# Performance work log

Hardware: AMD Instinct MI355X
Metric: run time of the kernel (lower is better)

## Reference

```python
import jax, jax.numpy as jnp
import numpy as np

B, T, D_MODEL = 4, 1024, 1024
H, DQK, DV = 16, 64, 64
POS_NUM = 2 * T - 1  # 2047
SCALE = 0.05  # keep softmax logits in a sane range for random weights


def setup_inputs() -> dict:
    key = jax.random.key(0)
    ks = jax.random.split(key, 8)
    x = jax.random.normal(ks[0], (B, T, D_MODEL), dtype=jnp.float32)
    W_Q = jax.random.normal(ks[1], (H, DQK, DQK), dtype=jnp.float32) * SCALE
    W_K = jax.random.normal(ks[2], (H, DQK, DQK), dtype=jnp.float32) * SCALE
    W_V = jax.random.normal(ks[3], (H, DQK, DV), dtype=jnp.float32) * SCALE
    W_Z = jax.random.normal(ks[4], (H * DV, D_MODEL), dtype=jnp.float32) * SCALE
    pos_K_emb = jax.random.normal(ks[5], (POS_NUM, DQK), dtype=jnp.float32) * SCALE
    pos_V_emb = jax.random.normal(ks[6], (POS_NUM, DV), dtype=jnp.float32) * SCALE
    mask = jnp.zeros((T, T), dtype=jnp.float32)  # additive attention mask
    pos = jax.random.randint(ks[7], (T, T), 0, POS_NUM, dtype=jnp.int32)
    return {"x": x, "W_Q": W_Q, "W_K": W_K, "W_V": W_V, "W_Z": W_Z,
            "pos_K_emb": pos_K_emb, "pos_V_emb": pos_V_emb,
            "mask": mask, "pos": pos}


def reference(x, W_Q, W_K, W_V, W_Z, pos_K_emb, pos_V_emb, mask, pos):
    Bs, Ts, _ = x.shape
    h, dqk, dv = W_V.shape
    # [B,T,D] -> [B,H,T,dQK]
    xh = x.reshape(Bs, Ts, h, dqk).transpose(0, 2, 1, 3)
    Q = jnp.einsum('bhtd,hde->bhte', xh, W_Q)
    K = jnp.einsum('bhtd,hde->bhte', xh, W_K)
    V = jnp.einsum('bhtd,hde->bhte', xh, W_V)
    # content scores + relative-position key bias
    PK = pos_K_emb[pos]                       # [T,T,dQK]
    scores = jnp.einsum('bhqd,bhkd->bhqk', Q, K)
    scores = scores + jnp.einsum('bhqd,qkd->bhqk', Q, PK)
    # NOTE: original adds mask BEFORE dividing by sqrt(dQK); replicate exactly
    scores = (scores + mask) / jnp.sqrt(jnp.asarray(dqk, dtype=scores.dtype))
    attn = jax.nn.softmax(scores, axis=-1)    # [B,H,T,T]
    ctx = jnp.einsum('bhqk,bhkd->bhqd', attn, V)
    PV = pos_V_emb[pos]                       # [T,T,dV]
    ctx = ctx + jnp.einsum('bhqk,qkd->bhqd', attn, PV)
    out = ctx.transpose(0, 2, 1, 3).reshape(Bs, Ts, h * dv)
    return out @ W_Z
```

## Files before the change

### kernel.cpp

```cpp
#include <hip/hip_runtime.h>
#include <hip/hip_bf16.h>

#define BB 4
#define TT 1024
#define DM 1024
#define HH 16

typedef __attribute__((ext_vector_type(8))) short short8;
typedef __attribute__((ext_vector_type(4))) short short4v;
typedef __attribute__((ext_vector_type(4))) float f32x4;
typedef __hip_bfloat16 bf16;
typedef unsigned char u8;

__device__ __forceinline__ f32x4 mfma16(short8 a, short8 b, f32x4 c) {
  return __builtin_amdgcn_mfma_f32_16x16x32_bf16(a, b, c, 0, 0, 0);
}
__device__ __forceinline__ f32x4 mfma8(long a, long b, f32x4 c) {
  return __builtin_amdgcn_mfma_f32_16x16x32_fp8_fp8(a, b, c, 0, 0, 0);
}

__global__ __launch_bounds__(256) void xb_kernel(
    const float* __restrict__ x, bf16* __restrict__ xb) {
  const size_t i = ((size_t)blockIdx.x * 256 + threadIdx.x) * 8;
  bf16 tmp[8];
#pragma unroll
  for (int j = 0; j < 8; ++j) tmp[j] = __float2bfloat16(x[i + j]);
  *(short8*)(xb + i) = *(const short8*)tmp;
}

__global__ __launch_bounds__(256) void pack_pm_kernel(
    const int* __restrict__ pos, const float* __restrict__ maskp,
    unsigned* __restrict__ pm) {
  const size_t i = (size_t)blockIdx.x * 256 + threadIdx.x;
  const unsigned mb = __float_as_uint(maskp[i]) & 0xffff0000u;
  pm[i] = mb | (unsigned)pos[i];
}

__global__ __launch_bounds__(256) void prep_w_kernel(
    const float* __restrict__ WQ, const float* __restrict__ WK,
    const float* __restrict__ WV, bf16* __restrict__ Wt) {
  __shared__ bf16 tl[64][72];
  const int h = blockIdx.x, m = blockIdx.y;
  const float* W = (m == 0 ? WQ : (m == 1 ? WK : WV)) + h * 4096;
  const int tid = threadIdx.x;
  const int r = tid >> 2, c = (tid & 3) * 16;
#pragma unroll
  for (int i = 0; i < 16; ++i)
    tl[r][c + i] = __float2bfloat16(W[r * 64 + c + i]);
  __syncthreads();
  bf16* o = Wt + ((size_t)(m * 16 + h) * 64 + r) * 64 + c;
#pragma unroll
  for (int i = 0; i < 16; ++i) o[i] = tl[c + i][r];
}

__global__ __launch_bounds__(256) void prep_posk8_kernel(
    const float* __restrict__ posK, u8* __restrict__ posK8) {
  const int idx = (blockIdx.x * 256 + threadIdx.x) * 2;
  const int p = idx >> 6, d = idx & 63;
  const float v0 = (p < 2047) ? posK[(size_t)p * 64 + d] : 0.f;
  const float v1 = (p < 2047) ? posK[(size_t)p * 64 + d + 1] : 0.f;
  const int pk = __builtin_amdgcn_cvt_pk_fp8_f32(v0, v1, 0, false);
  *(unsigned short*)(posK8 + idx) = (unsigned short)(pk & 0xffff);
}

__global__ __launch_bounds__(256) void trans_wz_kernel(
    const float* __restrict__ Wz, bf16* __restrict__ WzT) {
  __shared__ bf16 tile[64][72];
  const int k0 = blockIdx.y * 64, n0 = blockIdx.x * 64;
  const int tid = threadIdx.x;
  const int r = tid >> 2, c = (tid & 3) * 16;
  const float* s = Wz + (size_t)(k0 + r) * 1024 + n0 + c;
#pragma unroll
  for (int i = 0; i < 16; ++i) tile[r][c + i] = __float2bfloat16(s[i]);
  __syncthreads();
  const int n = tid >> 2;
  bf16* o = WzT + (size_t)(n0 + n) * 1024 + k0 + c;
#pragma unroll
  for (int i = 0; i < 16; ++i) o[i] = tile[c + i][n];
}

__global__ __launch_bounds__(256) void trans_v_kernel(
    const bf16* __restrict__ src, bf16* __restrict__ dst) {
  __shared__ bf16 tile[64][72];
  const int bh = blockIdx.y, t0 = blockIdx.x * 64;
  const int tid = threadIdx.x;
  const int r = tid >> 2, c = (tid & 3) * 16;
  const bf16* s = src + ((size_t)bh * TT + t0 + r) * 64 + c;
  *(short8*)(&tile[r][c]) = *(const short8*)(s);
  *(short8*)(&tile[r][c + 8]) = *(const short8*)(s + 8);
  __syncthreads();
  const int d = tid >> 2;
  bf16* o = dst + ((size_t)bh * 64 + d) * TT + t0 + c;
#pragma unroll
  for (int i = 0; i < 16; ++i) o[i] = tile[c + i][d];
}

__global__ __launch_bounds__(256) void qkv_mfma_kernel(
    const bf16* __restrict__ xb, const bf16* __restrict__ Wt,
    u8* __restrict__ Q8, u8* __restrict__ K8, bf16* __restrict__ Vg) {
  __shared__ __align__(16) bf16 xs[64 * 72];
  const int bh = blockIdx.y;
  const int b = bh >> 4, h = bh & 15;
  const int t0 = blockIdx.x * 64;
  const int tid = threadIdx.x;
  const int w = tid >> 6, lane = tid & 63, l15 = lane & 15, hi = lane >> 4;

  {
    const int r = tid >> 2, c = (tid & 3) * 16;
    const bf16* src = xb + ((size_t)b * TT + t0 + r) * DM + h * 64 + c;
    *(short8*)(xs + r * 72 + c) = *(const short8*)(src);
    *(short8*)(xs + r * 72 + c + 8) = *(const short8*)(src + 8);
  }
  __syncthreads();

  f32x4 aQ[4] = {{0.f, 0.f, 0.f, 0.f}, {0.f, 0.f, 0.f, 0.f},
                 {0.f, 0.f, 0.f, 0.f}, {0.f, 0.f, 0.f, 0.f}};
  f32x4 aK[4] = {{0.f, 0.f, 0.f, 0.f}, {0.f, 0.f, 0.f, 0.f},
                 {0.f, 0.f, 0.f, 0.f}, {0.f, 0.f, 0.f, 0.f}};
  f32x4 aV[4] = {{0.f, 0.f, 0.f, 0.f}, {0.f, 0.f, 0.f, 0.f},
                 {0.f, 0.f, 0.f, 0.f}, {0.f, 0.f, 0.f, 0.f}};
  const bf16* WtQ = Wt + (size_t)h * 4096;
  const bf16* WtK = Wt + (size_t)(16 + h) * 4096;
  const bf16* WtV = Wt + (size_t)(32 + h) * 4096;
#pragma unroll
  for (int kc = 0; kc < 2; ++kc) {
    const short8 a =
        *(const short8*)(xs + (w * 16 + l15) * 72 + kc * 32 + hi * 8);
#pragma unroll
    for (int nt = 0; nt < 4; ++nt) {
      const size_t wo = (size_t)(nt * 16 + l15) * 64 + kc * 32 + hi * 8;
      aQ[nt] = mfma16(a, *(const short8*)(WtQ + wo), aQ[nt]);
      aK[nt] = mfma16(a, *(const short8*)(WtK + wo), aK[nt]);
      aV[nt] = mfma16(a, *(const short8*)(WtV + wo), aV[nt]);
    }
  }
  const int t = t0 + w * 16 + hi * 4;
#pragma unroll
  for (int nt = 0; nt < 4; ++nt) {
#pragma unroll
    for (int j = 0; j < 4; ++j) {
      const size_t o = ((size_t)bh * TT + t + j) * 64 + nt * 16 + l15;
      Vg[o] = __float2bfloat16(aV[nt][j]);
    }
    const size_t o0 = ((size_t)bh * TT + t) * 64 + nt * 16 + l15;
    {
      const int p01 = __builtin_amdgcn_cvt_pk_fp8_f32(aQ[nt][0], aQ[nt][1], 0, false);
      const int p23 = __builtin_amdgcn_cvt_pk_fp8_f32(aQ[nt][2], aQ[nt][3], 0, false);
      Q8[o0] = (u8)(p01 & 0xff);
      Q8[o0 + 64] = (u8)((p01 >> 8) & 0xff);
      Q8[o0 + 128] = (u8)(p23 & 0xff);
      Q8[o0 + 192] = (u8)((p23 >> 8) & 0xff);
    }
    {
      const int p01 = __builtin_amdgcn_cvt_pk_fp8_f32(aK[nt][0], aK[nt][1], 0, false);
      const int p23 = __builtin_amdgcn_cvt_pk_fp8_f32(aK[nt][2], aK[nt][3], 0, false);
      K8[o0] = (u8)(p01 & 0xff);
      K8[o0 + 64] = (u8)((p01 >> 8) & 0xff);
      K8[o0 + 128] = (u8)(p23 & 0xff);
      K8[o0 + 192] = (u8)((p23 >> 8) & 0xff);
    }
  }
}

#define QP8_S 2052
#define PSM_S 72

__global__ __launch_bounds__(256, 1) void score_pv_kernel(
    const u8* __restrict__ Q8,
    const u8* __restrict__ K8,
    const u8* __restrict__ posK8,
    const bf16* __restrict__ Vt,
    const unsigned* __restrict__ pm,
    bf16* __restrict__ Pws,
    float* __restrict__ l_ws,
    float* __restrict__ ctxU,
    int slab) {
  __shared__ __align__(16) u8 QPsh[64 * QP8_S];
  __shared__ __align__(16) bf16 Psm[2][64 * PSM_S];
  __shared__ float lred[4][64];

  const int bh = blockIdx.x;
  const int qt = blockIdx.y;
  const int qlocal0 = qt * 64;
  const int qg0 = slab * 256 + qlocal0;
  const int tid = threadIdx.x;
  const int w = tid >> 6;
  const int lane = tid & 63;
  const int l15 = lane & 15;
  const int hi = lane >> 4;

  long aqA[4], aqB[4];
#pragma unroll
  for (int h = 0; h < 4; ++h) {
    const u8* Qrow =
        Q8 + ((size_t)bh * TT + qg0 + h * 16 + l15) * 64;
    aqA[h] = *(const long*)(Qrow + hi * 8);
    aqB[h] = *(const long*)(Qrow + 32 + hi * 8);
  }

  {
    const u8* Kp0 = posK8 + (size_t)(w * 32 * 16 + l15) * 64;
    long qb0 = *(const long*)(Kp0 + hi * 8);
    long qb1 = *(const long*)(Kp0 + 32 + hi * 8);
    for (int i = 0; i < 32; ++i) {
      const int pt = w * 32 + i;
      const long cb0 = qb0, cb1 = qb1;
      {
        const int ptn = w * 32 + ((i + 1) & 31);
        const u8* Kpn = posK8 + (size_t)(ptn * 16 + l15) * 64;
        qb0 = *(const long*)(Kpn + hi * 8);
        qb1 = *(const long*)(Kpn + 32 + hi * 8);
      }
      const int off = pt * 16 + l15;
#pragma unroll
      for (int h = 0; h < 4; ++h) {
        f32x4 a4 = {0.f, 0.f, 0.f, 0.f};
        a4 = mfma8(aqA[h], cb0, a4);
        a4 = mfma8(aqB[h], cb1, a4);
        const int p01 = __builtin_amdgcn_cvt_pk_fp8_f32(a4[0], a4[1], 0, false);
        const int p23 = __builtin_amdgcn_cvt_pk_fp8_f32(a4[2], a4[3], 0, false);
        const int qr = h * 16 + hi * 4;
        QPsh[(qr + 0) * QP8_S + off] = (u8)(p01 & 0xff);
        QPsh[(qr + 1) * QP8_S + off] = (u8)((p01 >> 8) & 0xff);
        QPsh[(qr + 2) * QP8_S + off] = (u8)(p23 & 0xff);
        QPsh[(qr + 3) * QP8_S + off] = (u8)((p23 >> 8) & 0xff);
      }
    }
  }
  __syncthreads();

  f32x4 acc[4] = {{0.f, 0.f, 0.f, 0.f}, {0.f, 0.f, 0.f, 0.f},
                  {0.f, 0.f, 0.f, 0.f}, {0.f, 0.f, 0.f, 0.f}};
  float lp[16];
#pragma unroll
  for (int j = 0; j < 16; ++j) lp[j] = 0.f;
  const int kk = w * 16 + l15;
  const u8* K8bh = K8 + (size_t)bh * TT * 64;
  const bf16* Vtrow = Vt + ((size_t)bh * 64 + w * 16 + l15) * TT;

  long nb0 = *(const long*)(K8bh + (size_t)kk * 64 + hi * 8);
  long nb1 = *(const long*)(K8bh + (size_t)kk * 64 + 32 + hi * 8);
  short8 nv0 = *(const short8*)(Vtrow + hi * 8);
  short8 nv1 = *(const short8*)(Vtrow + 32 + hi * 8);
  unsigned npm[16];
#pragma unroll
  for (int h = 0; h < 4; ++h)
#pragma unroll
    for (int j = 0; j < 4; ++j)
      npm[h * 4 + j] = pm[(size_t)(qg0 + h * 16 + hi * 4 + j) * TT + kk];

  for (int it = 0; it < 16; ++it) {
    const int k0 = it * 64;
    bf16* PsmC = &Psm[it & 1][0];
    const long cb0 = nb0, cb1 = nb1;
    const short8 cv0 = nv0, cv1 = nv1;
    unsigned cpm[16];
#pragma unroll
    for (int j = 0; j < 16; ++j) cpm[j] = npm[j];
    {
      const int k0n = ((it + 1) & 15) * 64;
      nb0 = *(const long*)(K8bh + (size_t)(k0n + kk) * 64 + hi * 8);
      nb1 = *(const long*)(K8bh + (size_t)(k0n + kk) * 64 + 32 + hi * 8);
      nv0 = *(const short8*)(Vtrow + k0n + hi * 8);
      nv1 = *(const short8*)(Vtrow + k0n + 32 + hi * 8);
#pragma unroll
      for (int h = 0; h < 4; ++h)
#pragma unroll
        for (int j = 0; j < 4; ++j)
          npm[h * 4 + j] =
              pm[(size_t)(qg0 + h * 16 + hi * 4 + j) * TT + k0n + kk];
    }
#pragma unroll
    for (int h = 0; h < 4; ++h) {
      f32x4 s = {0.f, 0.f, 0.f, 0.f};
      s = mfma8(aqA[h], cb0, s);
      s = mfma8(aqB[h], cb1, s);
#pragma unroll
      for (int j = 0; j < 4; ++j) {
        const int q = h * 16 + hi * 4 + j;
        const unsigned pmv = cpm[h * 4 + j];
        const float qp = __builtin_amdgcn_cvt_f32_fp8(
            (int)QPsh[q * QP8_S + (pmv & 0xffffu)], 0);
        const float sv =
            (s[j] + qp + __uint_as_float(pmv & 0xffff0000u)) * 0.125f;
        const float pe = __expf(sv);
        lp[h * 4 + j] += pe;
        PsmC[q * PSM_S + kk] = __float2bfloat16(pe);
      }
    }
    __syncthreads();
    {
      const int r = tid >> 2, c = (tid & 3) * 16;
      *(short8*)(Pws + ((size_t)(qlocal0 + r) * 64 + bh) * TT + k0 + c) =
          *(const short8*)(PsmC + r * PSM_S + c);
      *(short8*)(Pws + ((size_t)(qlocal0 + r) * 64 + bh) * TT + k0 + c + 8) =
          *(const short8*)(PsmC + r * PSM_S + c + 8);
    }
#pragma unroll
    for (int h = 0; h < 4; ++h) {
      const short8 pa0 =
          *(const short8*)(PsmC + (h * 16 + l15) * PSM_S + hi * 8);
      acc[h] = mfma16(pa0, cv0, acc[h]);
      const short8 pa1 =
          *(const short8*)(PsmC + (h * 16 + l15) * PSM_S + 32 + hi * 8);
      acc[h] = mfma16(pa1, cv1, acc[h]);
    }
  }

#pragma unroll
  for (int j = 0; j < 16; ++j) {
    float v = lp[j];
    v += __shfl_xor(v, 1);
    v += __shfl_xor(v, 2);
    v += __shfl_xor(v, 4);
    v += __shfl_xor(v, 8);
    lp[j] = v;
  }
  __syncthreads();
  if (l15 == 0) {
#pragma unroll
    for (int h = 0; h < 4; ++h)
#pragma unroll
      for (int j = 0; j < 4; ++j) lred[w][h * 16 + hi * 4 + j] = lp[h * 4 + j];
  }
  __syncthreads();
  if (tid < 64) {
    const float l = lred[0][tid] + lred[1][tid] + lred[2][tid] + lred[3][tid];
    l_ws[(size_t)bh * TT + qg0 + tid] = l;
  }
  {
    const int b = bh >> 4, h16 = bh & 15;
#pragma unroll
    for (int h = 0; h < 4; ++h)
#pragma unroll
      for (int j = 0; j < 4; ++j) {
        const int q = h * 16 + hi * 4 + j;
        ctxU[((size_t)b * TT + qg0 + q) * DM + h16 * 64 + w * 16 + l15] =
            acc[h][j];
      }
  }
}

#define PVT_S 72
__global__ __launch_bounds__(256) void pv_part_kernel(
    const bf16* __restrict__ Pws,
    const float* __restrict__ posV,
    const unsigned* __restrict__ pm,
    float* __restrict__ PP,
    int slab) {
  __shared__ __align__(16) bf16 PVt[2][64 * PVT_S];
  __shared__ unsigned short possh[256];

  const int qlocal = blockIdx.x;
  const int q = slab * 256 + qlocal;
  const int ks = blockIdx.y;
  const int kbase = ks * 256;
  const int tid = threadIdx.x;
  const int w = tid >> 6, lane = tid & 63, l15 = lane & 15, hi = lane >> 4;

  possh[tid] = (unsigned short)(pm[(size_t)q * TT + kbase + tid] & 0xffffu);
  __syncthreads();

  f32x4 acc[4] = {{0.f, 0.f, 0.f, 0.f}, {0.f, 0.f, 0.f, 0.f},
                  {0.f, 0.f, 0.f, 0.f}, {0.f, 0.f, 0.f, 0.f}};
  const bf16* Prow = Pws + ((size_t)qlocal * 64 + w * 16 + l15) * TT;

  for (int it = 0; it < 4; ++it) {
    const int k0 = kbase + it * 64;
    bf16* pvt = &PVt[it & 1][0];
    {
      const int kr = lane;
      const int dc = w * 16;
      const int p = possh[it * 64 + kr];
      const float* src = posV + (size_t)p * 64 + dc;
#pragma unroll
      for (int ii = 0; ii < 16; ii += 4) {
        const f32x4 v = *(const f32x4*)(src + ii);
        pvt[(dc + ii + 0) * PVT_S + kr] = __float2bfloat16(v[0]);
        pvt[(dc + ii + 1) * PVT_S + kr] = __float2bfloat16(v[1]);
        pvt[(dc + ii + 2) * PVT_S + kr] = __float2bfloat16(v[2]);
        pvt[(dc + ii + 3) * PVT_S + kr] = __float2bfloat16(v[3]);
      }
    }
    __syncthreads();
#pragma unroll
    for (int kc = 0; kc < 2; ++kc) {
      const short8 a = *(const short8*)(Prow + k0 + kc * 32 + hi * 8);
#pragma unroll
      for (int nt = 0; nt < 4; ++nt) {
        const short8 bv =
            *(const short8*)(pvt + (nt * 16 + l15) * PVT_S + kc * 32 + hi * 8);
        acc[nt] = mfma16(a, bv, acc[nt]);
      }
    }
  }

  const int bh0 = w * 16 + hi * 4;
#pragma unroll
  for (int j = 0; j < 4; ++j) {
    const int bh = bh0 + j;
    float* o = PP + (((size_t)ks * 256 + qlocal) * 64 + bh) * 64;
#pragma unroll
    for (int nt = 0; nt < 4; ++nt) o[nt * 16 + l15] = acc[nt][j];
  }
}

__global__ __launch_bounds__(256) void norm_kernel(
    const float* __restrict__ PP,
    const float* __restrict__ ctxU,
    const float* __restrict__ l_ws,
    bf16* __restrict__ ctxB,
    int slab) {
  const int i4 = blockIdx.x * 256 + threadIdx.x;
  const int e0 = i4 * 4;
  const int dm = e0 & 1023;
  const int qlocal = (e0 >> 10) & 255;
  const int b = e0 >> 18;
  const int h = dm >> 6, d0 = dm & 63;
  const int bh = b * 16 + h;
  const int q = slab * 256 + qlocal;

  f32x4 v = *(const f32x4*)(ctxU + ((size_t)b * TT + q) * DM + dm);
#pragma unroll
  for (int ks = 0; ks < 4; ++ks)
    v += *(const f32x4*)(PP + (((size_t)ks * 256 + qlocal) * 64 + bh) * 64 + d0);
  const float invl = 1.0f / l_ws[(size_t)bh * TT + q];
  bf16 o[4];
#pragma unroll
  for (int j = 0; j < 4; ++j) o[j] = __float2bfloat16(v[j] * invl);
  *(short4v*)(ctxB + ((size_t)b * TT + q) * DM + dm) = *(const short4v*)o;
}

__global__ __launch_bounds__(256) void outproj_mfma_kernel(
    const bf16* __restrict__ A,
    const bf16* __restrict__ Bt,
    float* __restrict__ C) {
  __shared__ __align__(16) bf16 As[128 * 72];
  __shared__ __align__(16) bf16 Bs[128 * 72];
  const int n0 = blockIdx.x * 128;
  const int m0 = blockIdx.y * 128;
  const int tid = threadIdx.x;
  const int w = tid >> 6, lane = tid & 63, l15 = lane & 15, hi = lane >> 4;
  const int wm = w >> 1, wn = w & 1;

  f32x4 acc[4][4];
#pragma unroll
  for (int i = 0; i < 4; ++i)
#pragma unroll
    for (int j = 0; j < 4; ++j) acc[i][j] = (f32x4){0.f, 0.f, 0.f, 0.f};

  const int sr = tid >> 1, sc = (tid & 1) * 32;
  for (int k0 = 0; k0 < 1024; k0 += 64) {
    __syncthreads();
    {
      const bf16* as = A + (size_t)(m0 + sr) * 1024 + k0 + sc;
      const bf16* bs = Bt + (size_t)(n0 + sr) * 1024 + k0 + sc;
#pragma unroll
      for (int ii = 0; ii < 32; ii += 8) {
        *(short8*)(As + sr * 72 + sc + ii) = *(const short8*)(as + ii);
        *(short8*)(Bs + sr * 72 + sc + ii) = *(const short8*)(bs + ii);
      }
    }
    __syncthreads();
#pragma unroll
    for (int kc = 0; kc < 2; ++kc) {
      short8 a[4], b[4];
#pragma unroll
      for (int i = 0; i < 4; ++i)
        a[i] = *(const short8*)(As + (wm * 64 + i * 16 + l15) * 72 + kc * 32 +
                                hi * 8);
#pragma unroll
      for (int j = 0; j < 4; ++j)
        b[j] = *(const short8*)(Bs + (wn * 64 + j * 16 + l15) * 72 + kc * 32 +
                                hi * 8);
#pragma unroll
      for (int i = 0; i < 4; ++i)
#pragma unroll
        for (int j = 0; j < 4; ++j) acc[i][j] = mfma16(a[i], b[j], acc[i][j]);
    }
  }
#pragma unroll
  for (int i = 0; i < 4; ++i) {
#pragma unroll
    for (int jj = 0; jj < 4; ++jj) {
      const size_t row = (size_t)(m0 + wm * 64 + i * 16 + hi * 4 + jj) * 1024;
#pragma unroll
      for (int j = 0; j < 4; ++j)
        C[row + n0 + wn * 64 + j * 16 + l15] = acc[i][j][jj];
    }
  }
}

extern "C" void kernel_launch(void* const* d_in, const int* in_sizes, int n_in,
                              void* d_out, int out_size, void* d_ws,
                              size_t ws_size, hipStream_t stream) {
  const float* x = (const float*)d_in[0];
  const float* WQ = (const float*)d_in[1];
  const float* WK = (const float*)d_in[2];
  const float* WV = (const float*)d_in[3];
  const float* WZ = (const float*)d_in[4];
  const float* posK = (const float*)d_in[5];
  const float* posV = (const float*)d_in[6];
  const float* maskp = (const float*)d_in[7];
  const int* pos = (const int*)d_in[8];
  float* out = (float*)d_out;

  char* p = (char*)d_ws;
  u8* Q8 = (u8*)p;            p += (size_t)64 * 1024 * 64;
  u8* K8 = (u8*)p;            p += (size_t)64 * 1024 * 64;
  bf16* Vb = (bf16*)p;        p += (size_t)64 * 1024 * 64 * 2;
  bf16* Vt = (bf16*)p;        p += (size_t)64 * 64 * 1024 * 2;
  u8* posK8 = (u8*)p;         p += (size_t)2048 * 64;
  bf16* WzT = (bf16*)p;       p += (size_t)1024 * 1024 * 2;
  bf16* Pws = (bf16*)p;       p += (size_t)256 * 64 * 1024 * 2;
  float* l_ws = (float*)p;    p += (size_t)64 * 1024 * 4;
  float* ctxU = (float*)p;    p += (size_t)4 * 1024 * 1024 * 4;
  bf16* ctxB = (bf16*)p;      p += (size_t)4 * 1024 * 1024 * 2;
  float* PP = (float*)p;      p += (size_t)4 * 256 * 64 * 64 * 4;
  unsigned* pm_ws = (unsigned*)p; p += (size_t)1024 * 1024 * 4;

  bf16* xb = (bf16*)ctxU;
  bf16* Wt = ctxB;

  xb_kernel<<<2048, 256, 0, stream>>>(x, xb);
  pack_pm_kernel<<<4096, 256, 0, stream>>>(pos, maskp, pm_ws);
  prep_w_kernel<<<dim3(16, 3), 256, 0, stream>>>(WQ, WK, WV, Wt);
  prep_posk8_kernel<<<256, 256, 0, stream>>>(posK, posK8);
  trans_wz_kernel<<<dim3(16, 16), 256, 0, stream>>>(WZ, WzT);
  qkv_mfma_kernel<<<dim3(16, 64), 256, 0, stream>>>(xb, Wt, Q8, K8, Vb);
  trans_v_kernel<<<dim3(16, 64), 256, 0, stream>>>(Vb, Vt);

  for (int slab = 0; slab < 4; ++slab) {
    score_pv_kernel<<<dim3(64, 4), 256, 0, stream>>>(
        Q8, K8, posK8, Vt, pm_ws, Pws, l_ws, ctxU, slab);
    pv_part_kernel<<<dim3(256, 4), 256, 0, stream>>>(Pws, posV, pm_ws, PP,
                                                     slab);
    norm_kernel<<<1024, 256, 0, stream>>>(PP, ctxU, l_ws, ctxB, slab);
  }
  outproj_mfma_kernel<<<dim3(8, 32), 256, 0, stream>>>(ctxB, WzT, out);
}
```

Baseline: 281.1 us.

## Split score_pv key range across two wave groups with 512-thread blocks

Doubles the score_pv block to 512 threads. The two 4-wave groups each handle half of the key range, using their own Psm buffer in place of double buffering, and the posK precompute is shared across all 8 waves. Partial PV accumulators are reduced through shared memory reused from QPsh before ctxU is written. This aims to raise the number of waves per CU, since the grid has only 256 blocks with one block per CU. The cost is an extra barrier per iteration and the shared-memory reduction.

```diff
diff --git a/kernel.cpp b/kernel.cpp
--- a/kernel.cpp
+++ b/kernel.cpp
@@ -163,9 +163,9 @@
 }
 
 #define QP8_S 2052
-#define PSM_S 72
-
-__global__ __launch_bounds__(256, 1) void score_pv_kernel(
+#define PSM_S 68
+
+__global__ __launch_bounds__(512, 1) void score_pv_kernel(
     const u8* __restrict__ Q8,
     const u8* __restrict__ K8,
     const u8* __restrict__ posK8,
@@ -177,36 +177,38 @@
     int slab) {
   __shared__ __align__(16) u8 QPsh[64 * QP8_S];
   __shared__ __align__(16) bf16 Psm[2][64 * PSM_S];
-  __shared__ float lred[4][64];
+  __shared__ float lred[8][64];
 
   const int bh = blockIdx.x;
   const int qt = blockIdx.y;
   const int qlocal0 = qt * 64;
   const int qg0 = slab * 256 + qlocal0;
   const int tid = threadIdx.x;
-  const int w = tid >> 6;
+  const int w8 = tid >> 6;
+  const int kg = w8 >> 2;
+  const int w = w8 & 3;
   const int lane = tid & 63;
   const int l15 = lane & 15;
   const int hi = lane >> 4;
+  const int ltid = tid & 255;
 
   long aqA[4], aqB[4];
 #pragma unroll
   for (int h = 0; h < 4; ++h) {
-    const u8* Qrow =
-        Q8 + ((size_t)bh * TT + qg0 + h * 16 + l15) * 64;
+    const u8* Qrow = Q8 + ((size_t)bh * TT + qg0 + h * 16 + l15) * 64;
     aqA[h] = *(const long*)(Qrow + hi * 8);
     aqB[h] = *(const long*)(Qrow + 32 + hi * 8);
   }
 
   {
-    const u8* Kp0 = posK8 + (size_t)(w * 32 * 16 + l15) * 64;
+    const u8* Kp0 = posK8 + (size_t)(w8 * 16 * 16 + l15) * 64;
     long qb0 = *(const long*)(Kp0 + hi * 8);
     long qb1 = *(const long*)(Kp0 + 32 + hi * 8);
-    for (int i = 0; i < 32; ++i) {
-      const int pt = w * 32 + i;
+    for (int i = 0; i < 16; ++i) {
+      const int pt = w8 * 16 + i;
       const long cb0 = qb0, cb1 = qb1;
       {
-        const int ptn = w * 32 + ((i + 1) & 31);
+        const int ptn = w8 * 16 + ((i + 1) & 15);
         const u8* Kpn = posK8 + (size_t)(ptn * 16 + l15) * 64;
         qb0 = *(const long*)(Kpn + hi * 8);
         qb1 = *(const long*)(Kpn + 32 + hi * 8);
@@ -234,33 +236,35 @@
   float lp[16];
 #pragma unroll
   for (int j = 0; j < 16; ++j) lp[j] = 0.f;
-  const int kk = w * 16 + l15;
+  const int kb = kg * 512;
+  const int ksl = w * 16 + l15;
   const u8* K8bh = K8 + (size_t)bh * TT * 64;
   const bf16* Vtrow = Vt + ((size_t)bh * 64 + w * 16 + l15) * TT;
-
-  long nb0 = *(const long*)(K8bh + (size_t)kk * 64 + hi * 8);
-  long nb1 = *(const long*)(K8bh + (size_t)kk * 64 + 32 + hi * 8);
-  short8 nv0 = *(const short8*)(Vtrow + hi * 8);
-  short8 nv1 = *(const short8*)(Vtrow + 32 + hi * 8);
+  bf16* PsmG = &Psm[kg][0];
+
+  long nb0 = *(const long*)(K8bh + (size_t)(kb + ksl) * 64 + hi * 8);
+  long nb1 = *(const long*)(K8bh + (size_t)(kb + ksl) * 64 + 32 + hi * 8);
+  short8 nv0 = *(const short8*)(Vtrow + kb + hi * 8);
+  short8 nv1 = *(const short8*)(Vtrow + kb + 32 + hi * 8);
   unsigned npm[16];
 #pragma unroll
   for (int h = 0; h < 4; ++h)
 #pragma unroll
     for (int j = 0; j < 4; ++j)
-      npm[h * 4 + j] = pm[(size_t)(qg0 + h * 16 + hi * 4 + j) * TT + kk];
-
-  for (int it = 0; it < 16; ++it) {
-    const int k0 = it * 64;
-    bf16* PsmC = &Psm[it & 1][0];
+      npm[h * 4 + j] =
+          pm[(size_t)(qg0 + h * 16 + hi * 4 + j) * TT + kb + ksl];
+
+  for (int it = 0; it < 8; ++it) {
+    const int k0 = kb + it * 64;
     const long cb0 = nb0, cb1 = nb1;
     const short8 cv0 = nv0, cv1 = nv1;
     unsigned cpm[16];
 #pragma unroll
     for (int j = 0; j < 16; ++j) cpm[j] = npm[j];
     {
-      const int k0n = ((it + 1) & 15) * 64;
-      nb0 = *(const long*)(K8bh + (size_t)(k0n + kk) * 64 + hi * 8);
-      nb1 = *(const long*)(K8bh + (size_t)(k0n + kk) * 64 + 32 + hi * 8);
+      const int k0n = kb + ((it + 1) & 7) * 64;
+      nb0 = *(const long*)(K8bh + (size_t)(k0n + ksl) * 64 + hi * 8);
+      nb1 = *(const long*)(K8bh + (size_t)(k0n + ksl) * 64 + 32 + hi * 8);
       nv0 = *(const short8*)(Vtrow + k0n + hi * 8);
       nv1 = *(const short8*)(Vtrow + k0n + 32 + hi * 8);
 #pragma unroll
@@ -268,7 +272,7 @@
 #pragma unroll
         for (int j = 0; j < 4; ++j)
           npm[h * 4 + j] =
-              pm[(size_t)(qg0 + h * 16 + hi * 4 + j) * TT + k0n + kk];
+              pm[(size_t)(qg0 + h * 16 + hi * 4 + j) * TT + k0n + ksl];
     }
 #pragma unroll
     for (int h = 0; h < 4; ++h) {
@@ -285,26 +289,27 @@
             (s[j] + qp + __uint_as_float(pmv & 0xffff0000u)) * 0.125f;
         const float pe = __expf(sv);
         lp[h * 4 + j] += pe;
-        PsmC[q * PSM_S + kk] = __float2bfloat16(pe);
+        PsmG[q * PSM_S + ksl] = __float2bfloat16(pe);
       }
     }
     __syncthreads();
     {
-      const int r = tid >> 2, c = (tid & 3) * 16;
+      const int r = ltid >> 2, c = (ltid & 3) * 16;
       *(short8*)(Pws + ((size_t)(qlocal0 + r) * 64 + bh) * TT + k0 + c) =
-          *(const short8*)(PsmC + r * PSM_S + c);
+          *(const short8*)(PsmG + r * PSM_S + c);
       *(short8*)(Pws + ((size_t)(qlocal0 + r) * 64 + bh) * TT + k0 + c + 8) =
-          *(const short8*)(PsmC + r * PSM_S + c + 8);
+          *(const short8*)(PsmG + r * PSM_S + c + 8);
     }
 #pragma unroll
     for (int h = 0; h < 4; ++h) {
       const short8 pa0 =
-          *(const short8*)(PsmC + (h * 16 + l15) * PSM_S + hi * 8);
+          *(const short8*)(PsmG + (h * 16 + l15) * PSM_S + hi * 8);
       acc[h] = mfma16(pa0, cv0, acc[h]);
       const short8 pa1 =
-          *(const short8*)(PsmC + (h * 16 + l15) * PSM_S + 32 + hi * 8);
+          *(const short8*)(PsmG + (h * 16 + l15) * PSM_S + 32 + hi * 8);
       acc[h] = mfma16(pa1, cv1, acc[h]);
     }
+    __syncthreads();
   }
 
 #pragma unroll
@@ -316,28 +321,33 @@
     v += __shfl_xor(v, 8);
     lp[j] = v;
   }
-  __syncthreads();
   if (l15 == 0) {
 #pragma unroll
     for (int h = 0; h < 4; ++h)
 #pragma unroll
-      for (int j = 0; j < 4; ++j) lred[w][h * 16 + hi * 4 + j] = lp[h * 4 + j];
-  }
+      for (int j = 0; j < 4; ++j)
+        lred[w8][h * 16 + hi * 4 + j] = lp[h * 4 + j];
+  }
+  float* red = (float*)QPsh;
+#pragma unroll
+  for (int h = 0; h < 4; ++h)
+#pragma unroll
+    for (int j = 0; j < 4; ++j)
+      red[(kg * 64 + h * 16 + hi * 4 + j) * PSM_S + w * 16 + l15] = acc[h][j];
   __syncthreads();
   if (tid < 64) {
-    const float l = lred[0][tid] + lred[1][tid] + lred[2][tid] + lred[3][tid];
+    float l = 0.f;
+#pragma unroll
+    for (int ww = 0; ww < 8; ++ww) l += lred[ww][tid];
     l_ws[(size_t)bh * TT + qg0 + tid] = l;
   }
   {
     const int b = bh >> 4, h16 = bh & 15;
-#pragma unroll
-    for (int h = 0; h < 4; ++h)
-#pragma unroll
-      for (int j = 0; j < 4; ++j) {
-        const int q = h * 16 + hi * 4 + j;
-        ctxU[((size_t)b * TT + qg0 + q) * DM + h16 * 64 + w * 16 + l15] =
-            acc[h][j];
-      }
+    for (int i = tid; i < 4096; i += 512) {
+      const int q = i >> 6, d = i & 63;
+      ctxU[((size_t)b * TT + qg0 + q) * DM + h16 * 64 + d] =
+          red[q * PSM_S + d] + red[(64 + q) * PSM_S + d];
+    }
   }
 }
 
@@ -531,7 +541,7 @@
   trans_v_kernel<<<dim3(16, 64), 256, 0, stream>>>(Vb, Vt);
 
   for (int slab = 0; slab < 4; ++slab) {
-    score_pv_kernel<<<dim3(64, 4), 256, 0, stream>>>(
+    score_pv_kernel<<<dim3(64, 4), 512, 0, stream>>>(
         Q8, K8, posK8, Vt, pm_ws, Pws, l_ws, ctxU, slab);
     pv_part_kernel<<<dim3(256, 4), 256, 0, stream>>>(Pws, posV, pm_ws, PP,
                                                      slab);
```

Result: slower. 317.2 us (+12.9%).
